# Kernel tuning notes

Measured on AMD Instinct MI355X. Metric: run time of the kernel, lower is better.

Reference implementation:

```python
import jax, jax.numpy as jnp
import numpy as np
from jax import lax

BATCH, SEQ_LEN, HIDDEN, CLASSES = 512, 256, 1024, 128

def _xavier(key, shape):
    fan_out, fan_in = shape
    std = float(np.sqrt(2.0 / (fan_in + fan_out)))
    return jax.random.normal(key, shape, dtype=jnp.float32) * std

def setup_inputs() -> dict:
    key = jax.random.key(0)
    k_x, k_hx, k_hh, k_ph = jax.random.split(key, 4)
    return {
        "x": jax.random.normal(k_x, (BATCH, SEQ_LEN), dtype=jnp.float32),
        "W_hx": _xavier(k_hx, (HIDDEN, 1)),
        "W_hh": _xavier(k_hh, (HIDDEN, HIDDEN)),
        "b_h": jnp.zeros((HIDDEN,), dtype=jnp.float32),
        "W_ph": _xavier(k_ph, (CLASSES, HIDDEN)),
        "b_p": jnp.zeros((CLASSES,), dtype=jnp.float32),
    }

def reference(x, W_hx, W_hh, b_h, W_ph, b_p):
    # x: [B, T] (input_dim == 1 per timestep, as in the torch module)
    B = x.shape[0]
    H = W_hh.shape[0]
    h0 = jnp.zeros((B, H), dtype=x.dtype)

    def step(h, xt):
        # xt: [B]; xt[:, None] @ W_hx.T -> [B, H]
        h_new = jnp.tanh(xt[:, None] @ W_hx.T + h @ W_hh.T + b_h)
        return h_new, None

    h_last, _ = lax.scan(step, h0, x.T)  # scan over time: x.T is [T, B]
    # Output head applied to final hidden state (loop's last p in torch code)
    return h_last @ W_ph.T + b_p  # [B, num_classes]
```

## Files before the change

kernel.cpp:

```cpp
#include <hip/hip_runtime.h>
#include <stdint.h>


#define BATCH 512
#define SEQ   256
#define HID   1024
#define CLS   128

#define GB 16
#define GJ 16
#define BT 32
#define JT 64
#define KC 256
#define WSTR 1028
#define SSTR 260
#define HSTR 68
#define SMEM_BYTES ((JT * WSTR + BT * SSTR) * 2)
#define HBUF_HALVES (BATCH * HID)
#define RED_OFF 2176

typedef __attribute__((ext_vector_type(8))) short  bf16x8;
typedef __attribute__((ext_vector_type(4))) short  s16x4;
typedef __attribute__((ext_vector_type(4))) float  f32x4;
typedef __attribute__((ext_vector_type(4))) int    i32x4;
typedef __attribute__((ext_vector_type(2))) unsigned int u32x2;

__device__ __forceinline__ unsigned short f2bf(float f) {
  unsigned int u = __float_as_uint(f);
  u = (u + 0x7FFFu + ((u >> 16) & 1u)) >> 16;
  return (unsigned short)u;
}
__device__ __forceinline__ float b2f(short h) {
  return __uint_as_float(((unsigned int)(unsigned short)h) << 16);
}

__device__ __forceinline__ void store_flag(int* p, int v) {
  asm volatile("global_store_dword %0, %1, off sc0 sc1" :: "v"(p), "v"(v) : "memory");
}
__device__ __forceinline__ int load_flag(const int* p) {
  int v;
  asm volatile("global_load_dword %0, %1, off sc0 sc1\n\t"
               "s_waitcnt vmcnt(0)" : "=v"(v) : "v"(p) : "memory");
  return v;
}
__device__ __forceinline__ void store16(void* p, i32x4 v) {
  asm volatile("global_store_dwordx4 %0, %1, off sc0 sc1" :: "v"(p), "v"(v) : "memory");
}
__device__ __forceinline__ void waitcnt0() {
  asm volatile("s_waitcnt vmcnt(0)" ::: "memory");
}
__device__ __forceinline__ void barrier_lgkm() {
  asm volatile("s_waitcnt lgkmcnt(0)\n\ts_barrier" ::: "memory");
}
__device__ __forceinline__ void issue4(const void* p, i32x4& a, i32x4& b, i32x4& c, i32x4& d) {
  asm volatile(
    "global_load_dwordx4 %0, %4, off sc0 sc1\n\t"
    "global_load_dwordx4 %1, %4, off offset:128 sc0 sc1\n\t"
    "global_load_dwordx4 %2, %4, off offset:256 sc0 sc1\n\t"
    "global_load_dwordx4 %3, %4, off offset:384 sc0 sc1"
    : "=&v"(a), "=&v"(b), "=&v"(c), "=&v"(d)
    : "v"(p) : "memory");
}
#define DEF_WAIT(NAME, N) \
__device__ __forceinline__ void NAME(i32x4& a, i32x4& b, i32x4& c, i32x4& d) { \
  asm volatile("s_waitcnt vmcnt(" #N ")" : "+v"(a), "+v"(b), "+v"(c), "+v"(d) :: "memory"); \
}
DEF_WAIT(wait_vm12, 12)
DEF_WAIT(wait_vm8, 8)
DEF_WAIT(wait_vm4, 4)
DEF_WAIT(wait_vm0, 0)

__device__ __forceinline__ void wr16(short* p, i32x4 v) {
  u32x2 lo, hi;
  lo.x = (unsigned)v.x; lo.y = (unsigned)v.y;
  hi.x = (unsigned)v.z; hi.y = (unsigned)v.w;
  *(u32x2*)p = lo;
  *(u32x2*)(p + 4) = hi;
}
__device__ __forceinline__ bf16x8 ld8(const short* p) {
  union { bf16x8 v8; s16x4 h[2]; } u;
  u.h[0] = *(const s16x4*)p;
  u.h[1] = *(const s16x4*)(p + 4);
  return u.v8;
}
__device__ __forceinline__ float tanh_fast(float z) {
  float e = __expf(2.f * z);
  return 1.f - 2.f / (e + 1.f);
}

__device__ __forceinline__ void mfma_chunk22(const short* sW, const short* sS,
                                             int cp, int kh, int l15, int quad, int c,
                                             f32x4& a00, f32x4& a01,
                                             f32x4& a10, f32x4& a11) {
  const short* B0  = sW + (cp * 32 + l15) * WSTR + c * KC + kh * 128 + quad * 8;
  const short* B1  = B0 + 16 * WSTR;
  const short* Ar0 = sS + l15 * SSTR + kh * 128 + quad * 8;
  const short* Ar1 = Ar0 + 16 * SSTR;
#pragma unroll
  for (int i = 0; i < 4; ++i) {
    bf16x8 b0 = ld8(B0  + i * 32);
    bf16x8 b1 = ld8(B1  + i * 32);
    bf16x8 a0 = ld8(Ar0 + i * 32);
    bf16x8 a1 = ld8(Ar1 + i * 32);
    a00 = __builtin_amdgcn_mfma_f32_16x16x32_bf16(a0, b0, a00, 0, 0, 0);
    a10 = __builtin_amdgcn_mfma_f32_16x16x32_bf16(a1, b0, a10, 0, 0, 0);
    a01 = __builtin_amdgcn_mfma_f32_16x16x32_bf16(a0, b1, a01, 0, 0, 0);
    a11 = __builtin_amdgcn_mfma_f32_16x16x32_bf16(a1, b1, a11, 0, 0, 0);
  }
}

__global__ void __launch_bounds__(256, 1)
rnn_persistent(const float* __restrict__ x, const float* __restrict__ Whx,
               const float* __restrict__ Whh, const float* __restrict__ bh,
               const float* __restrict__ Wph, const float* __restrict__ bp,
               float* __restrict__ out, unsigned short* hbuf, int* flags)
{
  extern __shared__ short smem[];
  short* sW = smem;
  short* sS = smem + JT * WSTR;

  const int tid  = threadIdx.x;
  const int bg   = blockIdx.x & 15;
  const int jg   = blockIdx.x >> 4;
  const int lane = tid & 63;
  const int wv   = tid >> 6;
  const int l15  = lane & 15;
  const int quad = lane >> 4;
  const int cp   = wv & 1;
  const int kh   = wv >> 1;

  {
    const int jr = tid >> 2;
    const int kq = tid & 3;
    const float* src = Whh + (jg * JT + jr) * HID + kq * 256;
    short* dst = sW + jr * WSTR + kq * 256;
#pragma unroll 4
    for (int i = 0; i < 64; ++i) {
      float4 f = *(const float4*)(src + i * 4);
      s16x4 h4;
      h4.x = (short)f2bf(f.x); h4.y = (short)f2bf(f.y);
      h4.z = (short)f2bf(f.z); h4.w = (short)f2bf(f.w);
      *(s16x4*)(dst + i * 4) = h4;
    }
  }

  const int j0 = jg * JT + cp * 32 + l15;
  const int j1 = j0 + 16;
  const float whx0 = Whx[j0], whx1 = Whx[j1];
  const float bhv0 = bh[j0],  bhv1 = bh[j1];
  const int grow0 = bg * BT + quad * 4;

  const int sr  = tid >> 3;
  const int seg = tid & 7;

  int* myflags = flags + bg * 64;

  for (int t = 0; t < SEQ; ++t) {
    const unsigned short* hin = hbuf + ((t + 1) & 1) * HBUF_HALVES;
    unsigned short*      hout = hbuf + (t & 1) * HBUF_HALVES;

    f32x4 acc00 = {0.f, 0.f, 0.f, 0.f};
    f32x4 acc01 = {0.f, 0.f, 0.f, 0.f};
    f32x4 acc10 = {0.f, 0.f, 0.f, 0.f};
    f32x4 acc11 = {0.f, 0.f, 0.f, 0.f};

    float xv0[4], xv1[4];
    {
      const float* xp = x + grow0 * SEQ + t;
#pragma unroll
      for (int rg = 0; rg < 4; ++rg) {
        xv0[rg] = xp[rg * SEQ];
        xv1[rg] = xp[(16 + rg) * SEQ];
      }
    }

    if (t > 0) {
      if (tid < GJ) {
        while (load_flag(myflags + tid) < t) {}
      }
      __syncthreads();

      const char* lbase = (const char*)(hin + (bg * BT + sr) * HID) + seg * 16;
      short* sdst = sS + sr * SSTR + seg * 8;

      i32x4 a0, a1, a2, a3, b0, b1, b2, b3, c0, c1, c2, c3, d0, d1, d2, d3;
      issue4(lbase,        a0, a1, a2, a3);
      issue4(lbase + 512,  b0, b1, b2, b3);
      issue4(lbase + 1024, c0, c1, c2, c3);
      issue4(lbase + 1536, d0, d1, d2, d3);

      wait_vm12(a0, a1, a2, a3);
      wr16(sdst, a0); wr16(sdst + 64, a1); wr16(sdst + 128, a2); wr16(sdst + 192, a3);
      barrier_lgkm();
      mfma_chunk22(sW, sS, cp, kh, l15, quad, 0, acc00, acc01, acc10, acc11);

      barrier_lgkm();
      wait_vm8(b0, b1, b2, b3);
      wr16(sdst, b0); wr16(sdst + 64, b1); wr16(sdst + 128, b2); wr16(sdst + 192, b3);
      barrier_lgkm();
      mfma_chunk22(sW, sS, cp, kh, l15, quad, 1, acc00, acc01, acc10, acc11);

      barrier_lgkm();
      wait_vm4(c0, c1, c2, c3);
      wr16(sdst, c0); wr16(sdst + 64, c1); wr16(sdst + 128, c2); wr16(sdst + 192, c3);
      barrier_lgkm();
      mfma_chunk22(sW, sS, cp, kh, l15, quad, 2, acc00, acc01, acc10, acc11);

      barrier_lgkm();
      wait_vm0(d0, d1, d2, d3);
      wr16(sdst, d0); wr16(sdst + 64, d1); wr16(sdst + 128, d2); wr16(sdst + 192, d3);
      barrier_lgkm();
      mfma_chunk22(sW, sS, cp, kh, l15, quad, 3, acc00, acc01, acc10, acc11);
    }

    barrier_lgkm();
    {
      float* red = (float*)(sS + RED_OFF);
      f32x4 w0 = kh ? acc00 : acc10;
      f32x4 w1 = kh ? acc01 : acc11;
      *(f32x4*)(red + tid * 8)     = w0;
      *(f32x4*)(red + tid * 8 + 4) = w1;
    }
    barrier_lgkm();
    {
      const float* red = (const float*)(sS + RED_OFF);
      const int ptid = tid ^ 128;
      f32x4 r0 = *(const f32x4*)(red + ptid * 8);
      f32x4 r1 = *(const f32x4*)(red + ptid * 8 + 4);
      f32x4 f0 = (kh ? acc10 : acc00) + r0;
      f32x4 f1 = (kh ? acc11 : acc01) + r1;

      short* hS = sS;
      const int rbase = kh * 16 + quad * 4;
#pragma unroll
      for (int rg = 0; rg < 4; ++rg) {
        float xr = kh ? xv1[rg] : xv0[rg];
        float z0 = f0[rg] + xr * whx0 + bhv0;
        hS[(rbase + rg) * HSTR + cp * 32 + l15] = (short)f2bf(tanh_fast(z0));
        float z1 = f1[rg] + xr * whx1 + bhv1;
        hS[(rbase + rg) * HSTR + cp * 32 + 16 + l15] = (short)f2bf(tanh_fast(z1));
      }
    }
    barrier_lgkm();
    {
      const short* hsrc = sS + sr * HSTR + seg * 8;
      u32x2 lo = *(const u32x2*)(hsrc);
      u32x2 hi = *(const u32x2*)(hsrc + 4);
      i32x4 sv; sv.x = (int)lo.x; sv.y = (int)lo.y; sv.z = (int)hi.x; sv.w = (int)hi.y;
      unsigned short* dst = hout + (bg * BT + sr) * HID + jg * JT + seg * 8;
      store16(dst, sv);
    }
    waitcnt0();
    barrier_lgkm();
    if (tid == 0) store_flag(myflags + jg, t + 1);
  }

  if (tid < GJ) {
    while (load_flag(myflags + tid) < SEQ) {}
  }
  __syncthreads();

  const unsigned short* hlast = hbuf + ((SEQ - 1) & 1) * HBUF_HALVES;
  const int cc = tid & 7;
  const int cg = jg * 8 + cc;
  const int hr = tid >> 3;
  float acc = 0.f;
  const char* lbase = (const char*)(hlast + (bg * BT + sr) * HID) + seg * 16;
  short* sdst = sS + sr * SSTR + seg * 8;
  for (int c = 0; c < 4; ++c) {
    __syncthreads();
    i32x4 p0, p1, p2, p3;
    issue4(lbase + c * 512, p0, p1, p2, p3);
    waitcnt0();
    wr16(sdst, p0); wr16(sdst + 64, p1); wr16(sdst + 128, p2); wr16(sdst + 192, p3);
    __syncthreads();
    const float* wp = Wph + cg * HID + c * KC;
    const short* hs = sS + hr * SSTR;
#pragma unroll 8
    for (int k4 = 0; k4 < 64; ++k4) {
      float4 w  = *(const float4*)(wp + k4 * 4);
      s16x4 hv  = *(const s16x4*)(hs + k4 * 4);
      acc += b2f(hv.x) * w.x + b2f(hv.y) * w.y + b2f(hv.z) * w.z + b2f(hv.w) * w.w;
    }
  }
  out[(bg * BT + hr) * CLS + cg] = acc + bp[cg];
}

extern "C" void kernel_launch(void* const* d_in, const int* in_sizes, int n_in,
                              void* d_out, int out_size, void* d_ws, size_t ws_size,
                              hipStream_t stream) {
  const float* x   = (const float*)d_in[0];
  const float* Whx = (const float*)d_in[1];
  const float* Whh = (const float*)d_in[2];
  const float* bh  = (const float*)d_in[3];
  const float* Wph = (const float*)d_in[4];
  const float* bp  = (const float*)d_in[5];
  float* out = (float*)d_out;

  unsigned short* hbuf = (unsigned short*)d_ws;
  int* flags = (int*)((char*)d_ws + (size_t)2 * HBUF_HALVES * 2);

  hipFuncSetAttribute(reinterpret_cast<const void*>(rnn_persistent),
                      hipFuncAttributeMaxDynamicSharedMemorySize, SMEM_BYTES);

  rnn_persistent<<<dim3(GB * GJ), dim3(256), SMEM_BYTES, stream>>>(
      x, Whx, Whh, bh, Wph, bp, out, hbuf, flags);
}
```

Before: 1.028 ms.

## Replace per-step flag barrier with parity tags embedded in hidden-state data

Drops the global flag array and the per-timestep spin-wait on flags. Instead, a parity tag is written into the low mantissa bit of the first element of each 16-byte segment of the bf16 hidden state. Readers check that bit and retry only when the data is stale, which removes a flag round trip and the store-drain wait before signalling. It also pads the reduction scratch layout to cut LDS bank conflicts. In exchange it perturbs some hidden values by one bf16 ulp, adds a memset of the workspace each launch, and its correctness relies on 16-byte stores being seen atomically.

New measurement: 1.115 ms. +8.4%, slower.

```diff
diff --git a/kernel.cpp b/kernel.cpp
--- a/kernel.cpp
+++ b/kernel.cpp
@@ -34,15 +34,6 @@
   return __uint_as_float(((unsigned int)(unsigned short)h) << 16);
 }
 
-__device__ __forceinline__ void store_flag(int* p, int v) {
-  asm volatile("global_store_dword %0, %1, off sc0 sc1" :: "v"(p), "v"(v) : "memory");
-}
-__device__ __forceinline__ int load_flag(const int* p) {
-  int v;
-  asm volatile("global_load_dword %0, %1, off sc0 sc1\n\t"
-               "s_waitcnt vmcnt(0)" : "=v"(v) : "v"(p) : "memory");
-  return v;
-}
 __device__ __forceinline__ void store16(void* p, i32x4 v) {
   asm volatile("global_store_dwordx4 %0, %1, off sc0 sc1" :: "v"(p), "v"(v) : "memory");
 }
@@ -86,6 +77,19 @@
 __device__ __forceinline__ float tanh_fast(float z) {
   float e = __expf(2.f * z);
   return 1.f - 2.f / (e + 1.f);
+}
+
+__device__ __forceinline__ bool stale4(const i32x4& a, const i32x4& b,
+                                       const i32x4& c, const i32x4& d, int tg) {
+  return ((((a.x ^ tg) | (b.x ^ tg) | (c.x ^ tg) | (d.x ^ tg)) & 1)) != 0;
+}
+__device__ __forceinline__ void retry4(const void* p, i32x4& a, i32x4& b,
+                                       i32x4& c, i32x4& d, int tg) {
+  do {
+    asm volatile("s_sleep 2" ::: "memory");
+    issue4(p, a, b, c, d);
+    waitcnt0();
+  } while (stale4(a, b, c, d, tg));
 }
 
 __device__ __forceinline__ void mfma_chunk22(const short* sW, const short* sS,
@@ -113,7 +117,7 @@
 rnn_persistent(const float* __restrict__ x, const float* __restrict__ Whx,
                const float* __restrict__ Whh, const float* __restrict__ bh,
                const float* __restrict__ Wph, const float* __restrict__ bp,
-               float* __restrict__ out, unsigned short* hbuf, int* flags)
+               float* __restrict__ out, unsigned short* hbuf)
 {
   extern __shared__ short smem[];
   short* sW = smem;
@@ -149,15 +153,20 @@
   const float whx0 = Whx[j0], whx1 = Whx[j1];
   const float bhv0 = bh[j0],  bhv1 = bh[j1];
   const int grow0 = bg * BT + quad * 4;
+  const int tagger = (l15 & 7) == 0;
 
   const int sr  = tid >> 3;
   const int seg = tid & 7;
 
-  int* myflags = flags + bg * 64;
+  const int roff  = tid * 8 + (tid >> 2) * 4;
+  const int ptid  = tid ^ 128;
+  const int proff = ptid * 8 + (ptid >> 2) * 4;
 
   for (int t = 0; t < SEQ; ++t) {
     const unsigned short* hin = hbuf + ((t + 1) & 1) * HBUF_HALVES;
     unsigned short*      hout = hbuf + (t & 1) * HBUF_HALVES;
+    const int tg_w = (t >> 1) & 1;
+    const int tg_r = ((t - 1) >> 1) & 1;
 
     f32x4 acc00 = {0.f, 0.f, 0.f, 0.f};
     f32x4 acc01 = {0.f, 0.f, 0.f, 0.f};
@@ -175,11 +184,6 @@
     }
 
     if (t > 0) {
-      if (tid < GJ) {
-        while (load_flag(myflags + tid) < t) {}
-      }
-      __syncthreads();
-
       const char* lbase = (const char*)(hin + (bg * BT + sr) * HID) + seg * 16;
       short* sdst = sS + sr * SSTR + seg * 8;
 
@@ -190,24 +194,44 @@
       issue4(lbase + 1536, d0, d1, d2, d3);
 
       wait_vm12(a0, a1, a2, a3);
+      if (__builtin_expect(stale4(a0, a1, a2, a3, tg_r), 0)) {
+        waitcnt0();
+        do {
+          asm volatile("s_sleep 2" ::: "memory");
+          issue4(lbase,        a0, a1, a2, a3);
+          issue4(lbase + 512,  b0, b1, b2, b3);
+          issue4(lbase + 1024, c0, c1, c2, c3);
+          issue4(lbase + 1536, d0, d1, d2, d3);
+          waitcnt0();
+        } while (stale4(a0, a1, a2, a3, tg_r));
+      }
       wr16(sdst, a0); wr16(sdst + 64, a1); wr16(sdst + 128, a2); wr16(sdst + 192, a3);
       barrier_lgkm();
       mfma_chunk22(sW, sS, cp, kh, l15, quad, 0, acc00, acc01, acc10, acc11);
 
       barrier_lgkm();
       wait_vm8(b0, b1, b2, b3);
+      if (__builtin_expect(stale4(b0, b1, b2, b3, tg_r), 0)) {
+        waitcnt0(); retry4(lbase + 512, b0, b1, b2, b3, tg_r);
+      }
       wr16(sdst, b0); wr16(sdst + 64, b1); wr16(sdst + 128, b2); wr16(sdst + 192, b3);
       barrier_lgkm();
       mfma_chunk22(sW, sS, cp, kh, l15, quad, 1, acc00, acc01, acc10, acc11);
 
       barrier_lgkm();
       wait_vm4(c0, c1, c2, c3);
+      if (__builtin_expect(stale4(c0, c1, c2, c3, tg_r), 0)) {
+        waitcnt0(); retry4(lbase + 1024, c0, c1, c2, c3, tg_r);
+      }
       wr16(sdst, c0); wr16(sdst + 64, c1); wr16(sdst + 128, c2); wr16(sdst + 192, c3);
       barrier_lgkm();
       mfma_chunk22(sW, sS, cp, kh, l15, quad, 2, acc00, acc01, acc10, acc11);
 
       barrier_lgkm();
       wait_vm0(d0, d1, d2, d3);
+      if (__builtin_expect(stale4(d0, d1, d2, d3, tg_r), 0)) {
+        retry4(lbase + 1536, d0, d1, d2, d3, tg_r);
+      }
       wr16(sdst, d0); wr16(sdst + 64, d1); wr16(sdst + 128, d2); wr16(sdst + 192, d3);
       barrier_lgkm();
       mfma_chunk22(sW, sS, cp, kh, l15, quad, 3, acc00, acc01, acc10, acc11);
@@ -218,15 +242,14 @@
       float* red = (float*)(sS + RED_OFF);
       f32x4 w0 = kh ? acc00 : acc10;
       f32x4 w1 = kh ? acc01 : acc11;
-      *(f32x4*)(red + tid * 8)     = w0;
-      *(f32x4*)(red + tid * 8 + 4) = w1;
+      *(f32x4*)(red + roff)     = w0;
+      *(f32x4*)(red + roff + 4) = w1;
     }
     barrier_lgkm();
     {
       const float* red = (const float*)(sS + RED_OFF);
-      const int ptid = tid ^ 128;
-      f32x4 r0 = *(const f32x4*)(red + ptid * 8);
-      f32x4 r1 = *(const f32x4*)(red + ptid * 8 + 4);
+      f32x4 r0 = *(const f32x4*)(red + proff);
+      f32x4 r1 = *(const f32x4*)(red + proff + 4);
       f32x4 f0 = (kh ? acc10 : acc00) + r0;
       f32x4 f1 = (kh ? acc11 : acc01) + r1;
 
@@ -235,10 +258,14 @@
 #pragma unroll
       for (int rg = 0; rg < 4; ++rg) {
         float xr = kh ? xv1[rg] : xv0[rg];
-        float z0 = f0[rg] + xr * whx0 + bhv0;
-        hS[(rbase + rg) * HSTR + cp * 32 + l15] = (short)f2bf(tanh_fast(z0));
-        float z1 = f1[rg] + xr * whx1 + bhv1;
-        hS[(rbase + rg) * HSTR + cp * 32 + 16 + l15] = (short)f2bf(tanh_fast(z1));
+        unsigned short v0 = f2bf(tanh_fast(f0[rg] + xr * whx0 + bhv0));
+        unsigned short v1 = f2bf(tanh_fast(f1[rg] + xr * whx1 + bhv1));
+        if (tagger) {
+          v0 = (unsigned short)((v0 & 0xFFFEu) | (unsigned)tg_w);
+          v1 = (unsigned short)((v1 & 0xFFFEu) | (unsigned)tg_w);
+        }
+        hS[(rbase + rg) * HSTR + cp * 32 + l15]      = (short)v0;
+        hS[(rbase + rg) * HSTR + cp * 32 + 16 + l15] = (short)v1;
       }
     }
     barrier_lgkm();
@@ -250,17 +277,11 @@
       unsigned short* dst = hout + (bg * BT + sr) * HID + jg * JT + seg * 8;
       store16(dst, sv);
     }
-    waitcnt0();
     barrier_lgkm();
-    if (tid == 0) store_flag(myflags + jg, t + 1);
   }
 
-  if (tid < GJ) {
-    while (load_flag(myflags + tid) < SEQ) {}
-  }
-  __syncthreads();
-
   const unsigned short* hlast = hbuf + ((SEQ - 1) & 1) * HBUF_HALVES;
+  const int tg_l = ((SEQ - 1) >> 1) & 1;
   const int cc = tid & 7;
   const int cg = jg * 8 + cc;
   const int hr = tid >> 3;
@@ -272,6 +293,7 @@
     i32x4 p0, p1, p2, p3;
     issue4(lbase + c * 512, p0, p1, p2, p3);
     waitcnt0();
+    if (stale4(p0, p1, p2, p3, tg_l)) retry4(lbase + c * 512, p0, p1, p2, p3, tg_l);
     wr16(sdst, p0); wr16(sdst + 64, p1); wr16(sdst + 128, p2); wr16(sdst + 192, p3);
     __syncthreads();
     const float* wp = Wph + cg * HID + c * KC;
@@ -298,11 +320,12 @@
   float* out = (float*)d_out;
 
   unsigned short* hbuf = (unsigned short*)d_ws;
-  int* flags = (int*)((char*)d_ws + (size_t)2 * HBUF_HALVES * 2);
+
+  hipMemsetAsync(d_ws, 0xFF, (size_t)2 * HBUF_HALVES * 2, stream);
 
   hipFuncSetAttribute(reinterpret_cast<const void*>(rnn_persistent),
                       hipFuncAttributeMaxDynamicSharedMemorySize, SMEM_BYTES);
 
   rnn_persistent<<<dim3(GB * GJ), dim3(256), SMEM_BYTES, stream>>>(
-      x, Whx, Whh, bh, Wph, bp, out, hbuf, flags);
-}
+      x, Whx, Whh, bh, Wph, bp, out, hbuf);
+}
```
